# Kernel tuning notes

Hardware: AMD Instinct MI355X
Metric: run time of the kernel (lower is better)

## Reference

```python
import jax, jax.numpy as jnp
import numpy as np

B, S, D = 8, 1024, 1024
H, DK = 16, 64  # heads, key_size (== head_size)
NEG = 1e12


def setup_inputs() -> dict:
    key = jax.random.key(0)
    ks = jax.random.split(key, 10)
    s = 1.0 / np.sqrt(D)
    return {
        "q": jax.random.normal(ks[0], (B, S, D), jnp.float32),
        "k": jax.random.normal(ks[1], (B, S, D), jnp.float32),
        "v": jax.random.normal(ks[2], (B, S, D), jnp.float32),
        "pos_bias": jax.random.normal(ks[3], (S, S, DK), jnp.float32) * 0.02,
        "Wq": jax.random.normal(ks[4], (D, H * DK), jnp.float32) * s,
        "Wk": jax.random.normal(ks[5], (D, H * DK), jnp.float32) * s,
        "Wv": jax.random.normal(ks[6], (D, H * DK), jnp.float32) * s,
        "Wo": jax.random.normal(ks[7], (H * DK, D), jnp.float32) * s,
        "bq": jnp.zeros((H * DK,), jnp.float32),
        "bk": jnp.zeros((H * DK,), jnp.float32),
        "bv": jnp.zeros((H * DK,), jnp.float32),
        "bo": jnp.zeros((D,), jnp.float32),
        "q_mask": jnp.ones((B, S), jnp.int32),
        "v_mask": jnp.ones((B, S), jnp.int32),
    }


def reference(q, k, v, pos_bias, Wq, Wk, Wv, Wo, bq, bk, bv, bo, q_mask, v_mask):
    qm = q_mask.astype(q.dtype)  # [B,Sq]
    vm = v_mask.astype(q.dtype)  # [B,Sk]
    # Projections (faithful quirk: K is projected from v, as in the source)
    qw = (q @ Wq + bq).reshape(B, S, H, DK)
    kw = (v @ Wk + bk).reshape(B, S, H, DK)
    vw = (v @ Wv + bv).reshape(B, S, H, DK)
    # scores + inline relative-position bias ('typial_relative' branch)
    a = jnp.einsum('bjhd,bkhd->bhjk', qw, kw)
    a = a + jnp.einsum('bjhd,jkd->bhjk', qw, pos_bias)
    a = a / jnp.sqrt(jnp.asarray(DK, a.dtype))
    # additive key mask, then softmax over keys
    a = a - (1.0 - vm)[:, None, None, :] * NEG
    a = jax.nn.softmax(a, axis=-1)
    o = jnp.einsum('bhjk,bkhd->bjhd', a, vw)  # [B,Sq,H,DK]
    o = o.reshape(B, S, H * DK) @ Wo + bo
    # multiplicative query mask on output
    o = o * qm[:, :, None]
    return o
```

## Files before the change

### kernel.cpp

```cpp
#include <hip/hip_runtime.h>

using short8 = __attribute__((ext_vector_type(8))) short;
using f32x4  = __attribute__((ext_vector_type(4))) float;
using u16x4  = __attribute__((ext_vector_type(4))) unsigned short;
using fl4    = __attribute__((ext_vector_type(4))) float;

#define MFMA16(a, b, c) __builtin_amdgcn_mfma_f32_16x16x32_bf16((a), (b), (c), 0, 0, 0)

static __device__ __forceinline__ unsigned short f2bf(float f) {
  union { float f; unsigned u; } x; x.f = f;
  return (unsigned short)((x.u + 0x7FFFu + ((x.u >> 16) & 1u)) >> 16);
}
static __device__ __forceinline__ float bf2f(unsigned short s) {
  union { unsigned u; float f; } x; x.u = ((unsigned)s) << 16;
  return x.f;
}

static __device__ __forceinline__ void gload16(const void* g, void* l) {
  __builtin_amdgcn_global_load_lds((const __attribute__((address_space(1))) void*)g,
                                   (__attribute__((address_space(3))) void*)l, 16, 0, 0);
}

__global__ __launch_bounds__(256) void k_wconv4(
    const float* __restrict__ W0, const float* __restrict__ W1,
    const float* __restrict__ W2, const float* __restrict__ W3,
    unsigned short* __restrict__ Wt0, unsigned short* __restrict__ Wt1,
    unsigned short* __restrict__ Wt2, unsigned short* __restrict__ Wt3) {
  const float* W = (blockIdx.z == 0) ? W0 : (blockIdx.z == 1) ? W1
                   : (blockIdx.z == 2) ? W2 : W3;
  unsigned short* Wt = (blockIdx.z == 0) ? Wt0 : (blockIdx.z == 1) ? Wt1
                       : (blockIdx.z == 2) ? Wt2 : Wt3;
  __shared__ float tile[64][65];
  const int t = threadIdx.x;
  const int n0 = blockIdx.x * 64, k0 = blockIdx.y * 64;
#pragma unroll
  for (int p = 0; p < 4; ++p) {
    int row = p * 16 + (t >> 4);
    int c4 = (t & 15) * 4;
    fl4 val = *(const fl4*)&W[(size_t)(k0 + row) * 1024 + n0 + c4];
    tile[row][c4 + 0] = val[0];
    tile[row][c4 + 1] = val[1];
    tile[row][c4 + 2] = val[2];
    tile[row][c4 + 3] = val[3];
  }
  __syncthreads();
#pragma unroll
  for (int p = 0; p < 4; ++p) {
    int n = p * 16 + (t >> 4);
    int k4 = (t & 15) * 4;
    u16x4 u;
    u[0] = f2bf(tile[k4 + 0][n]);
    u[1] = f2bf(tile[k4 + 1][n]);
    u[2] = f2bf(tile[k4 + 2][n]);
    u[3] = f2bf(tile[k4 + 3][n]);
    *(u16x4*)&Wt[(size_t)(n0 + n) * 1024 + k0 + k4] = u;
  }
}

__global__ __launch_bounds__(256) void k_cvt(const float* __restrict__ a,
                                             const float* __restrict__ b,
                                             unsigned short* __restrict__ oa,
                                             unsigned short* __restrict__ ob) {
  const float* src = blockIdx.y ? b : a;
  unsigned short* dst = blockIdx.y ? ob : oa;
  size_t i = ((size_t)blockIdx.x * 256 + threadIdx.x) * 8;
  fl4 v0 = *(const fl4*)&src[i];
  fl4 v1 = *(const fl4*)&src[i + 4];
  u16x4 u0, u1;
  u0[0] = f2bf(v0[0]); u0[1] = f2bf(v0[1]); u0[2] = f2bf(v0[2]); u0[3] = f2bf(v0[3]);
  u1[0] = f2bf(v1[0]); u1[1] = f2bf(v1[1]); u1[2] = f2bf(v1[2]); u1[3] = f2bf(v1[3]);
  *(u16x4*)&dst[i] = u0;
  *(u16x4*)&dst[i + 4] = u1;
}

__global__ __launch_bounds__(256) void k_proj2(
    const unsigned short* __restrict__ QB, const unsigned short* __restrict__ VB,
    const unsigned short* __restrict__ WtQ, const unsigned short* __restrict__ WtK,
    const unsigned short* __restrict__ WtV,
    const float* __restrict__ bq, const float* __restrict__ bk,
    const float* __restrict__ bv,
    unsigned short* __restrict__ QW, unsigned short* __restrict__ KW,
    unsigned short* __restrict__ VWT) {
  const int mode = blockIdx.z;
  const unsigned short* A8 = (mode == 0) ? QB : VB;
  const unsigned short* Wt = (mode == 0) ? WtQ : (mode == 1) ? WtK : WtV;
  const float* bias = (mode == 0) ? bq : (mode == 1) ? bk : bv;
  const int n0 = blockIdx.x * 128, m0 = blockIdx.y * 128;
  const int t = threadIdx.x, lane = t & 63, w = t >> 6;
  const int g = lane >> 4, ln = lane & 15;
  const int wm = w >> 1, wn = w & 1;
  __shared__ unsigned short sh[16896];
  unsigned short* As = sh;
  unsigned short* Bs = sh + 8192;
  const int srow = lane >> 3;
  const int scol = (lane & 7) * 8;
  f32x4 acc[4][4] = {};
  for (int kk = 0; kk < 1024; kk += 64) {
    __syncthreads();
#pragma unroll
    for (int p = 0; p < 4; ++p) {
      gload16(&A8[(size_t)(m0 + p * 32 + w * 8 + srow) * 1024 + kk + scol],
              &As[p * 2048 + w * 512]);
      gload16(&Wt[(size_t)(n0 + p * 32 + w * 8 + srow) * 1024 + kk + scol],
              &Bs[p * 2048 + w * 512]);
    }
    __syncthreads();
#pragma unroll
    for (int ks = 0; ks < 2; ++ks) {
      short8 af[4];
#pragma unroll
      for (int fm = 0; fm < 4; ++fm)
        af[fm] = *(const short8*)&As[(wm * 64 + fm * 16 + ln) * 64 + ks * 32 + 8 * g];
#pragma unroll
      for (int fn = 0; fn < 4; ++fn) {
        short8 bfr = *(const short8*)&Bs[(wn * 64 + fn * 16 + ln) * 64 + ks * 32 + 8 * g];
#pragma unroll
        for (int fm = 0; fm < 4; ++fm) acc[fm][fn] = MFMA16(af[fm], bfr, acc[fm][fn]);
      }
    }
  }
  __syncthreads();
  const float scale = (mode == 0) ? 0.125f : 1.0f;
#pragma unroll
  for (int fn = 0; fn < 4; ++fn) {
    float bn = bias[n0 + wn * 64 + fn * 16 + ln];
#pragma unroll
    for (int fm = 0; fm < 4; ++fm) {
#pragma unroll
      for (int r = 0; r < 4; ++r) {
        float val = (acc[fm][fn][r] + bn) * scale;
        sh[(wm * 64 + fm * 16 + 4 * g + r) * 132 + wn * 64 + fn * 16 + ln] = f2bf(val);
      }
    }
  }
  __syncthreads();
  if (mode < 2) {
    unsigned short* OUT = (mode == 0) ? QW : KW;
#pragma unroll
    for (int p = 0; p < 16; ++p) {
      int row = p * 8 + (t >> 5), c4 = (t & 31) * 4;
      *(u16x4*)&OUT[(size_t)(m0 + row) * 1024 + n0 + c4] =
          *(const u16x4*)&sh[row * 132 + c4];
    }
  } else {
    const int b = m0 >> 10, s0 = m0 & 1023;
#pragma unroll
    for (int p = 0; p < 16; ++p) {
#pragma unroll
      for (int qh = 0; qh < 2; ++qh) {
        int hdl = p * 8 + (t >> 5);
        int sl = qh * 64 + (t & 31) * 2;
        unsigned lo = sh[sl * 132 + hdl];
        unsigned hi = sh[(sl + 1) * 132 + hdl];
        int hd = n0 + hdl;
        int h = hd >> 6, d = hd & 63;
        *(unsigned*)&VWT[((size_t)(b * 16 + h) * 64 + d) * 1024 + s0 + sl] =
            lo | (hi << 16);
      }
    }
  }
}

__global__ __launch_bounds__(256) void k_pbias(
    const unsigned short* __restrict__ QW, const float* __restrict__ pb,
    const int* __restrict__ vmask, unsigned short* __restrict__ CB, int jbase) {
  const int kt = blockIdx.x;
  const int jl = blockIdx.y;
  const int j = jbase + jl;
  const int t = threadIdx.x, lane = t & 63, w = t >> 6;
  const int g = lane >> 4, ln = lane & 15;
  const int wm = w >> 1, wn = w & 1;
  __shared__ unsigned short sm[18432];
  unsigned short* a_lds = sm;
  unsigned short* b_lds = sm + 9216;
#pragma unroll
  for (int p = 0; p < 8; ++p) {
    int i4 = p * 256 + t;
    int row = i4 >> 4, c4 = (i4 & 15) * 4;
    *(u16x4*)&a_lds[row * 72 + c4] =
        *(const u16x4*)&QW[((size_t)(row >> 4) * 1024 + j) * 1024 + (row & 15) * 64 + c4];
  }
#pragma unroll
  for (int p = 0; p < 8; ++p) {
    int i4 = p * 256 + t;
    int row = i4 >> 4, c4 = (i4 & 15) * 4;
    fl4 val = *(const fl4*)&pb[((size_t)j * 1024 + kt * 128 + row) * 64 + c4];
    u16x4 u;
    u[0] = f2bf(val[0]); u[1] = f2bf(val[1]);
    u[2] = f2bf(val[2]); u[3] = f2bf(val[3]);
    *(u16x4*)&b_lds[row * 72 + c4] = u;
  }
  __syncthreads();
  f32x4 acc[4][4] = {};
#pragma unroll
  for (int ks = 0; ks < 2; ++ks) {
    short8 af[4];
#pragma unroll
    for (int fm = 0; fm < 4; ++fm)
      af[fm] = *(const short8*)&a_lds[(wm * 64 + fm * 16 + ln) * 72 + ks * 32 + 8 * g];
#pragma unroll
    for (int fn = 0; fn < 4; ++fn) {
      short8 bfr = *(const short8*)&b_lds[(wn * 64 + fn * 16 + ln) * 72 + ks * 32 + 8 * g];
#pragma unroll
      for (int fm = 0; fm < 4; ++fm) acc[fm][fn] = MFMA16(af[fm], bfr, acc[fm][fn]);
    }
  }
  __syncthreads();
#pragma unroll
  for (int fn = 0; fn < 4; ++fn) {
    int kcol = kt * 128 + wn * 64 + fn * 16 + ln;
#pragma unroll
    for (int fm = 0; fm < 4; ++fm) {
      float off = vmask[(wm * 4 + fm) * 1024 + kcol] ? 0.f : -1e12f;
#pragma unroll
      for (int r = 0; r < 4; ++r)
        sm[(wm * 64 + fm * 16 + 4 * g + r) * 132 + wn * 64 + fn * 16 + ln] =
            f2bf(acc[fm][fn][r] + off);
    }
  }
  __syncthreads();
#pragma unroll
  for (int p = 0; p < 16; ++p) {
    int row = p * 8 + (t >> 5), c4 = (t & 31) * 4;
    *(u16x4*)&CB[((size_t)row * 512 + jl) * 1024 + kt * 128 + c4] =
        *(const u16x4*)&sm[row * 132 + c4];
  }
}

__global__ __launch_bounds__(256) void k_attn(
    const unsigned short* __restrict__ QW, const unsigned short* __restrict__ KW,
    const unsigned short* __restrict__ VWT, const unsigned short* __restrict__ CB,
    unsigned short* __restrict__ OB, int jbase) {
  const int jt = blockIdx.x, h = blockIdx.y, b = blockIdx.z;
  const int t = threadIdx.x, lane = t & 63, w = t >> 6;
  const int g = lane >> 4, ln = lane & 15;
  const int j0 = jbase + jt * 64;
  const int jl0 = jt * 64;
  __shared__ unsigned short lds_k[128 * 72];
  __shared__ unsigned short lds_vt[64 * 136];
  __shared__ unsigned short lds_p[4 * 16 * 136];
  unsigned short* pw = &lds_p[w * (16 * 136)];
  short8 qf[2];
  {
    const size_t qrow = ((size_t)b * 1024 + (j0 + w * 16 + ln)) * 1024 + h * 64;
    qf[0] = *(const short8*)&QW[qrow + 8 * g];
    qf[1] = *(const short8*)&QW[qrow + 32 + 8 * g];
  }
  const size_t cb_row = ((size_t)(b * 16 + h) * 512 + jl0 + w * 16 + ln) * 1024;

  u16x4 rk[8], rv[8], rcb[8];
#define LOAD_KV(kt_)                                                              \
  {                                                                               \
    _Pragma("unroll") for (int p = 0; p < 8; ++p) {                               \
      int i4 = p * 256 + t;                                                       \
      int row = i4 >> 4, c4 = (i4 & 15) * 4;                                      \
      rk[p] = *(const u16x4*)&KW[((size_t)b * 1024 + (kt_) * 128 + row) * 1024 +  \
                                 h * 64 + c4];                                    \
    }                                                                             \
    _Pragma("unroll") for (int p = 0; p < 8; ++p) {                               \
      int i4 = p * 256 + t;                                                       \
      int row = i4 >> 5, c4 = (i4 & 31) * 4;                                      \
      rv[p] = *(const u16x4*)&VWT[(((size_t)b * 16 + h) * 64 + row) * 1024 +      \
                                  (kt_) * 128 + c4];                              \
    }                                                                             \
    _Pragma("unroll") for (int p = 0; p < 8; ++p)                                 \
        rcb[p] = *(const u16x4*)&CB[cb_row + (kt_) * 128 + p * 16 + 4 * g];       \
  }

  LOAD_KV(0);
  f32x4 o_acc[4] = {};
  float l_par = 0.f;

  for (int kt = 0; kt < 8; ++kt) {
    __syncthreads();
#pragma unroll
    for (int p = 0; p < 8; ++p) {
      int i4 = p * 256 + t;
      int row = i4 >> 4, c4 = (i4 & 15) * 4;
      *(u16x4*)&lds_k[row * 72 + c4] = rk[p];
    }
#pragma unroll
    for (int p = 0; p < 8; ++p) {
      int i4 = p * 256 + t;
      int row = i4 >> 5, c4 = (i4 & 31) * 4;
      *(u16x4*)&lds_vt[row * 136 + c4] = rv[p];
    }
    f32x4 s[8];
#pragma unroll
    for (int fm = 0; fm < 8; ++fm) {
#pragma unroll
      for (int r = 0; r < 4; ++r) s[fm][r] = bf2f(rcb[fm][r]);
    }
    if (kt < 7) LOAD_KV(kt + 1);
    __syncthreads();
#pragma unroll
    for (int ks = 0; ks < 2; ++ks) {
#pragma unroll
      for (int fm = 0; fm < 8; ++fm) {
        short8 af = *(const short8*)&lds_k[(fm * 16 + ln) * 72 + ks * 32 + 8 * g];
        s[fm] = MFMA16(af, qf[ks], s[fm]);
      }
    }
#pragma unroll
    for (int fm = 0; fm < 8; ++fm) {
      u16x4 pp;
#pragma unroll
      for (int r = 0; r < 4; ++r) {
        float pv = __expf(s[fm][r] - 12.0f);
        l_par += pv;
        pp[r] = f2bf(pv);
      }
      *(u16x4*)&pw[ln * 136 + fm * 16 + 4 * g] = pp;
    }
    asm volatile("s_waitcnt lgkmcnt(0)" ::: "memory");
#pragma unroll
    for (int ks = 0; ks < 4; ++ks) {
      short8 bp = *(const short8*)&pw[ln * 136 + ks * 32 + 8 * g];
#pragma unroll
      for (int fm = 0; fm < 4; ++fm) {
        short8 av = *(const short8*)&lds_vt[(fm * 16 + ln) * 136 + ks * 32 + 8 * g];
        o_acc[fm] = MFMA16(av, bp, o_acc[fm]);
      }
    }
  }
  l_par += __shfl_xor(l_par, 16);
  l_par += __shfl_xor(l_par, 32);
  float inv = 1.0f / l_par;
  const size_t orow = ((size_t)b * 1024 + (j0 + w * 16 + ln)) * 1024 + h * 64;
#pragma unroll
  for (int fm = 0; fm < 4; ++fm) {
    u16x4 uo;
#pragma unroll
    for (int r = 0; r < 4; ++r) uo[r] = f2bf(o_acc[fm][r] * inv);
    *(u16x4*)&OB[orow + fm * 16 + 4 * g] = uo;
  }
#undef LOAD_KV
}

__global__ __launch_bounds__(256) void k_out2(
    const unsigned short* __restrict__ OB, const unsigned short* __restrict__ WtO,
    const float* __restrict__ bo, const int* __restrict__ qmask,
    float* __restrict__ out) {
  const int n0 = blockIdx.x * 128, m0 = blockIdx.y * 128;
  const int t = threadIdx.x, lane = t & 63, w = t >> 6;
  const int g = lane >> 4, ln = lane & 15;
  const int wm = w >> 1, wn = w & 1;
  __shared__ unsigned short sh[16384];
  unsigned short* As = sh;
  unsigned short* Bs = sh + 8192;
  const int srow = lane >> 3;
  const int scol = (lane & 7) * 8;
  f32x4 acc[4][4] = {};
  for (int kk = 0; kk < 1024; kk += 64) {
    __syncthreads();
#pragma unroll
    for (int p = 0; p < 4; ++p) {
      gload16(&OB[(size_t)(m0 + p * 32 + w * 8 + srow) * 1024 + kk + scol],
              &As[p * 2048 + w * 512]);
      gload16(&WtO[(size_t)(n0 + p * 32 + w * 8 + srow) * 1024 + kk + scol],
              &Bs[p * 2048 + w * 512]);
    }
    __syncthreads();
#pragma unroll
    for (int ks = 0; ks < 2; ++ks) {
      short8 af[4];
#pragma unroll
      for (int fm = 0; fm < 4; ++fm)
        af[fm] = *(const short8*)&As[(wm * 64 + fm * 16 + ln) * 64 + ks * 32 + 8 * g];
#pragma unroll
      for (int fn = 0; fn < 4; ++fn) {
        short8 bfr = *(const short8*)&Bs[(wn * 64 + fn * 16 + ln) * 64 + ks * 32 + 8 * g];
#pragma unroll
        for (int fm = 0; fm < 4; ++fm) acc[fm][fn] = MFMA16(af[fm], bfr, acc[fm][fn]);
      }
    }
  }
  float bn[4];
#pragma unroll
  for (int fn = 0; fn < 4; ++fn) bn[fn] = bo[n0 + wn * 64 + fn * 16 + ln];
#pragma unroll
  for (int fm = 0; fm < 4; ++fm) {
#pragma unroll
    for (int r = 0; r < 4; ++r) {
      int row = m0 + wm * 64 + fm * 16 + 4 * g + r;
      float qm = (float)qmask[row];
#pragma unroll
      for (int fn = 0; fn < 4; ++fn)
        out[(size_t)row * 1024 + n0 + wn * 64 + fn * 16 + ln] =
            (acc[fm][fn][r] + bn[fn]) * qm;
    }
  }
}

extern "C" void kernel_launch(void* const* d_in, const int* in_sizes, int n_in,
                              void* d_out, int out_size, void* d_ws, size_t ws_size,
                              hipStream_t stream) {
  const float* q  = (const float*)d_in[0];
  const float* v  = (const float*)d_in[2];
  const float* pb = (const float*)d_in[3];
  const float* Wq = (const float*)d_in[4];
  const float* Wk = (const float*)d_in[5];
  const float* Wv = (const float*)d_in[6];
  const float* Wo = (const float*)d_in[7];
  const float* bq = (const float*)d_in[8];
  const float* bk = (const float*)d_in[9];
  const float* bv = (const float*)d_in[10];
  const float* bo = (const float*)d_in[11];
  const int* qm = (const int*)d_in[12];
  const int* vm = (const int*)d_in[13];
  float* out = (float*)d_out;

  unsigned short* ws = (unsigned short*)d_ws;
  const size_t M1 = 1024 * 1024;
  unsigned short* WTQ = ws;
  unsigned short* WTK = WTQ + M1;
  unsigned short* WTV = WTK + M1;
  unsigned short* WTO = WTV + M1;
  unsigned short* QB  = WTO + M1;
  unsigned short* VB  = QB + 8 * M1;
  unsigned short* QW  = VB + 8 * M1;
  unsigned short* KW  = QW + 8 * M1;
  unsigned short* VWT = KW + 8 * M1;
  unsigned short* OB  = VWT + 8 * M1;
  unsigned short* CB  = OB + 8 * M1;

  k_wconv4<<<dim3(16, 16, 4), 256, 0, stream>>>(Wq, Wk, Wv, Wo, WTQ, WTK, WTV, WTO);
  k_cvt<<<dim3(4096, 2), 256, 0, stream>>>(q, v, QB, VB);
  k_proj2<<<dim3(8, 64, 3), 256, 0, stream>>>(QB, VB, WTQ, WTK, WTV, bq, bk, bv,
                                              QW, KW, VWT);
  for (int st = 0; st < 2; ++st) {
    k_pbias<<<dim3(8, 512), 256, 0, stream>>>(QW, pb, vm, CB, st * 512);
    k_attn<<<dim3(8, 16, 8), 256, 0, stream>>>(QW, KW, VWT, CB, OB, st * 512);
  }
  k_out2<<<dim3(8, 64), 256, 0, stream>>>(OB, WTO, bo, qm, out);
}
```

Measured before the change: 390.4 us.

## Triple-buffer GEMM K-loop with swizzled LDS and use exp2 softmax

Replaces the synchronous two-barrier GEMM loop in the projection and output kernels with a shared macro. The macro keeps three LDS stages in flight through async global-to-LDS loads and uses vmcnt waits with one barrier per 32-wide K step, plus an XOR swizzle on LDS reads to reduce bank conflicts. The softmax now folds log2(e) into the Q scale and mask offset so it can call native v_exp_f32, and it uses packed bf16 conversion instructions. This adds LDS footprint, which may lower occupancy, and shifts the fixed softmax offset from 12 to 17 in the exp2 domain.

```diff
diff --git a/kernel.cpp b/kernel.cpp
--- a/kernel.cpp
+++ b/kernel.cpp
@@ -15,11 +15,20 @@
   union { unsigned u; float f; } x; x.u = ((unsigned)s) << 16;
   return x.f;
 }
+static __device__ __forceinline__ float fexp2(float x) {
+  float r; asm("v_exp_f32 %0, %1" : "=v"(r) : "v"(x)); return r;
+}
+static __device__ __forceinline__ unsigned pk2(float lo, float hi) {
+  unsigned r; asm("v_cvt_pk_bf16_f32 %0, %1, %2" : "=v"(r) : "v"(lo), "v"(hi));
+  return r;
+}
 
 static __device__ __forceinline__ void gload16(const void* g, void* l) {
   __builtin_amdgcn_global_load_lds((const __attribute__((address_space(1))) void*)g,
                                    (__attribute__((address_space(3))) void*)l, 16, 0, 0);
 }
+
+#define LOG2E 1.4426950408889634f
 
 __global__ __launch_bounds__(256) void k_wconv4(
     const float* __restrict__ W0, const float* __restrict__ W1,
@@ -73,7 +82,58 @@
   *(u16x4*)&dst[i + 4] = u1;
 }
 
-__global__ __launch_bounds__(256) void k_proj2(
+#define GEMM3_CORE(APTR, BPTR)                                                  \
+  const int t = threadIdx.x, lane = t & 63, w = t >> 6;                         \
+  const int g = lane >> 4, ln = lane & 15;                                      \
+  const int wm = w >> 1, wn = w & 1;                                            \
+  __shared__ unsigned short sh[24576];    \
+  const int srow = lane >> 2;                                                   \
+  const int sc = (lane & 3) ^ ((lane >> 3) & 3);                                \
+  const int rsw = ((ln >> 1) & 3);                                              \
+  f32x4 acc[4][4] = {};                                                         \
+  _Pragma("unroll") for (int pre = 0; pre < 2; ++pre) {                         \
+    _Pragma("unroll") for (int p = 0; p < 2; ++p) {                             \
+      gload16(&APTR[(size_t)(m0 + p * 64 + w * 16 + srow) * 1024 + pre * 32 + sc * 8], \
+              &sh[pre * 8192 + (p * 64 + w * 16) * 32]);                        \
+      gload16(&BPTR[(size_t)(n0 + p * 64 + w * 16 + srow) * 1024 + pre * 32 + sc * 8], \
+              &sh[pre * 8192 + 4096 + (p * 64 + w * 16) * 32]);                 \
+    }                                                                           \
+  }                                                                             \
+  int cur = 0;                                                                  \
+  for (int tt = 0; tt < 32; ++tt) {                                             \
+    if (tt < 31) {                                                              \
+      asm volatile("s_waitcnt vmcnt(4)" ::: "memory");                          \
+    } else {                                                                    \
+      asm volatile("s_waitcnt vmcnt(0)" ::: "memory");                          \
+    }                                                                           \
+    __builtin_amdgcn_sched_barrier(0);                                          \
+    __builtin_amdgcn_s_barrier();                                               \
+    __builtin_amdgcn_sched_barrier(0);                                          \
+    if (tt < 30) {                                                              \
+      int bb = cur + 2; if (bb >= 3) bb -= 3;                                   \
+      int kk = (tt + 2) * 32;                                                   \
+      _Pragma("unroll") for (int p = 0; p < 2; ++p) {                           \
+        gload16(&APTR[(size_t)(m0 + p * 64 + w * 16 + srow) * 1024 + kk + sc * 8], \
+                &sh[bb * 8192 + (p * 64 + w * 16) * 32]);                       \
+        gload16(&BPTR[(size_t)(n0 + p * 64 + w * 16 + srow) * 1024 + kk + sc * 8], \
+                &sh[bb * 8192 + 4096 + (p * 64 + w * 16) * 32]);                \
+      }                                                                         \
+    }                                                                           \
+    const unsigned short* As = &sh[cur * 8192];                                 \
+    const unsigned short* Bs = As + 4096;                                       \
+    short8 af[4], bfr[4];                                                       \
+    _Pragma("unroll") for (int fm = 0; fm < 4; ++fm)                            \
+        af[fm] = *(const short8*)&As[(wm * 64 + fm * 16 + ln) * 32 + (g ^ rsw) * 8]; \
+    _Pragma("unroll") for (int fn = 0; fn < 4; ++fn)                            \
+        bfr[fn] = *(const short8*)&Bs[(wn * 64 + fn * 16 + ln) * 32 + (g ^ rsw) * 8]; \
+    _Pragma("unroll") for (int fn = 0; fn < 4; ++fn) {                          \
+      _Pragma("unroll") for (int fm = 0; fm < 4; ++fm)                          \
+          acc[fm][fn] = MFMA16(af[fm], bfr[fn], acc[fm][fn]);                   \
+    }                                                                           \
+    cur = (cur == 2) ? 0 : cur + 1;                                             \
+  }
+
+__global__ __launch_bounds__(256) void k_proj3(
     const unsigned short* __restrict__ QB, const unsigned short* __restrict__ VB,
     const unsigned short* __restrict__ WtQ, const unsigned short* __restrict__ WtK,
     const unsigned short* __restrict__ WtV,
@@ -86,41 +146,9 @@
   const unsigned short* Wt = (mode == 0) ? WtQ : (mode == 1) ? WtK : WtV;
   const float* bias = (mode == 0) ? bq : (mode == 1) ? bk : bv;
   const int n0 = blockIdx.x * 128, m0 = blockIdx.y * 128;
-  const int t = threadIdx.x, lane = t & 63, w = t >> 6;
-  const int g = lane >> 4, ln = lane & 15;
-  const int wm = w >> 1, wn = w & 1;
-  __shared__ unsigned short sh[16896];
-  unsigned short* As = sh;
-  unsigned short* Bs = sh + 8192;
-  const int srow = lane >> 3;
-  const int scol = (lane & 7) * 8;
-  f32x4 acc[4][4] = {};
-  for (int kk = 0; kk < 1024; kk += 64) {
-    __syncthreads();
-#pragma unroll
-    for (int p = 0; p < 4; ++p) {
-      gload16(&A8[(size_t)(m0 + p * 32 + w * 8 + srow) * 1024 + kk + scol],
-              &As[p * 2048 + w * 512]);
-      gload16(&Wt[(size_t)(n0 + p * 32 + w * 8 + srow) * 1024 + kk + scol],
-              &Bs[p * 2048 + w * 512]);
-    }
-    __syncthreads();
-#pragma unroll
-    for (int ks = 0; ks < 2; ++ks) {
-      short8 af[4];
-#pragma unroll
-      for (int fm = 0; fm < 4; ++fm)
-        af[fm] = *(const short8*)&As[(wm * 64 + fm * 16 + ln) * 64 + ks * 32 + 8 * g];
-#pragma unroll
-      for (int fn = 0; fn < 4; ++fn) {
-        short8 bfr = *(const short8*)&Bs[(wn * 64 + fn * 16 + ln) * 64 + ks * 32 + 8 * g];
-#pragma unroll
-        for (int fm = 0; fm < 4; ++fm) acc[fm][fn] = MFMA16(af[fm], bfr, acc[fm][fn]);
-      }
-    }
-  }
-  __syncthreads();
-  const float scale = (mode == 0) ? 0.125f : 1.0f;
+  GEMM3_CORE(A8, Wt)
+  __syncthreads();
+  const float scale = (mode == 0) ? (0.125f * LOG2E) : 1.0f;
 #pragma unroll
   for (int fn = 0; fn < 4; ++fn) {
     float bn = bias[n0 + wn * 64 + fn * 16 + ln];
@@ -157,6 +185,29 @@
         *(unsigned*)&VWT[((size_t)(b * 16 + h) * 64 + d) * 1024 + s0 + sl] =
             lo | (hi << 16);
       }
+    }
+  }
+}
+
+__global__ __launch_bounds__(256) void k_out3(
+    const unsigned short* __restrict__ OB, const unsigned short* __restrict__ WtO,
+    const float* __restrict__ bo, const int* __restrict__ qmask,
+    float* __restrict__ out) {
+  const int n0 = blockIdx.x * 128, m0 = blockIdx.y * 128;
+  GEMM3_CORE(OB, WtO)
+  float bn[4];
+#pragma unroll
+  for (int fn = 0; fn < 4; ++fn) bn[fn] = bo[n0 + wn * 64 + fn * 16 + ln];
+#pragma unroll
+  for (int fm = 0; fm < 4; ++fm) {
+#pragma unroll
+    for (int r = 0; r < 4; ++r) {
+      int row = m0 + wm * 64 + fm * 16 + 4 * g + r;
+      float qm = (float)qmask[row];
+#pragma unroll
+      for (int fn = 0; fn < 4; ++fn)
+        out[(size_t)row * 1024 + n0 + wn * 64 + fn * 16 + ln] =
+            (acc[fm][fn][r] + bn[fn]) * qm;
     }
   }
 }
@@ -211,7 +262,7 @@
     int kcol = kt * 128 + wn * 64 + fn * 16 + ln;
 #pragma unroll
     for (int fm = 0; fm < 4; ++fm) {
-      float off = vmask[(wm * 4 + fm) * 1024 + kcol] ? 0.f : -1e12f;
+      float off = vmask[(wm * 4 + fm) * 1024 + kcol] ? 0.f : (-1e12f * LOG2E);
 #pragma unroll
       for (int r = 0; r < 4; ++r)
         sm[(wm * 64 + fm * 16 + 4 * g + r) * 132 + wn * 64 + fn * 16 + ln] =
@@ -303,14 +354,15 @@
     }
 #pragma unroll
     for (int fm = 0; fm < 8; ++fm) {
-      u16x4 pp;
-#pragma unroll
-      for (int r = 0; r < 4; ++r) {
-        float pv = __expf(s[fm][r] - 12.0f);
-        l_par += pv;
-        pp[r] = f2bf(pv);
-      }
-      *(u16x4*)&pw[ln * 136 + fm * 16 + 4 * g] = pp;
+      float pv0 = fexp2(s[fm][0] - 17.0f);
+      float pv1 = fexp2(s[fm][1] - 17.0f);
+      float pv2 = fexp2(s[fm][2] - 17.0f);
+      float pv3 = fexp2(s[fm][3] - 17.0f);
+      l_par += (pv0 + pv1) + (pv2 + pv3);
+      union { u16x4 v; unsigned u[2]; } pp;
+      pp.u[0] = pk2(pv0, pv1);
+      pp.u[1] = pk2(pv2, pv3);
+      *(u16x4*)&pw[ln * 136 + fm * 16 + 4 * g] = pp.v;
     }
     asm volatile("s_waitcnt lgkmcnt(0)" ::: "memory");
 #pragma unroll
@@ -329,67 +381,12 @@
   const size_t orow = ((size_t)b * 1024 + (j0 + w * 16 + ln)) * 1024 + h * 64;
 #pragma unroll
   for (int fm = 0; fm < 4; ++fm) {
-    u16x4 uo;
-#pragma unroll
-    for (int r = 0; r < 4; ++r) uo[r] = f2bf(o_acc[fm][r] * inv);
-    *(u16x4*)&OB[orow + fm * 16 + 4 * g] = uo;
+    union { u16x4 v; unsigned u[2]; } uo;
+    uo.u[0] = pk2(o_acc[fm][0] * inv, o_acc[fm][1] * inv);
+    uo.u[1] = pk2(o_acc[fm][2] * inv, o_acc[fm][3] * inv);
+    *(u16x4*)&OB[orow + fm * 16 + 4 * g] = uo.v;
   }
 #undef LOAD_KV
-}
-
-__global__ __launch_bounds__(256) void k_out2(
-    const unsigned short* __restrict__ OB, const unsigned short* __restrict__ WtO,
-    const float* __restrict__ bo, const int* __restrict__ qmask,
-    float* __restrict__ out) {
-  const int n0 = blockIdx.x * 128, m0 = blockIdx.y * 128;
-  const int t = threadIdx.x, lane = t & 63, w = t >> 6;
-  const int g = lane >> 4, ln = lane & 15;
-  const int wm = w >> 1, wn = w & 1;
-  __shared__ unsigned short sh[16384];
-  unsigned short* As = sh;
-  unsigned short* Bs = sh + 8192;
-  const int srow = lane >> 3;
-  const int scol = (lane & 7) * 8;
-  f32x4 acc[4][4] = {};
-  for (int kk = 0; kk < 1024; kk += 64) {
-    __syncthreads();
-#pragma unroll
-    for (int p = 0; p < 4; ++p) {
-      gload16(&OB[(size_t)(m0 + p * 32 + w * 8 + srow) * 1024 + kk + scol],
-              &As[p * 2048 + w * 512]);
-      gload16(&WtO[(size_t)(n0 + p * 32 + w * 8 + srow) * 1024 + kk + scol],
-              &Bs[p * 2048 + w * 512]);
-    }
-    __syncthreads();
-#pragma unroll
-    for (int ks = 0; ks < 2; ++ks) {
-      short8 af[4];
-#pragma unroll
-      for (int fm = 0; fm < 4; ++fm)
-        af[fm] = *(const short8*)&As[(wm * 64 + fm * 16 + ln) * 64 + ks * 32 + 8 * g];
-#pragma unroll
-      for (int fn = 0; fn < 4; ++fn) {
-        short8 bfr = *(const short8*)&Bs[(wn * 64 + fn * 16 + ln) * 64 + ks * 32 + 8 * g];
-#pragma unroll
-        for (int fm = 0; fm < 4; ++fm) acc[fm][fn] = MFMA16(af[fm], bfr, acc[fm][fn]);
-      }
-    }
-  }
-  float bn[4];
-#pragma unroll
-  for (int fn = 0; fn < 4; ++fn) bn[fn] = bo[n0 + wn * 64 + fn * 16 + ln];
-#pragma unroll
-  for (int fm = 0; fm < 4; ++fm) {
-#pragma unroll
-    for (int r = 0; r < 4; ++r) {
-      int row = m0 + wm * 64 + fm * 16 + 4 * g + r;
-      float qm = (float)qmask[row];
-#pragma unroll
-      for (int fn = 0; fn < 4; ++fn)
-        out[(size_t)row * 1024 + n0 + wn * 64 + fn * 16 + ln] =
-            (acc[fm][fn][r] + bn[fn]) * qm;
-    }
-  }
 }
 
 extern "C" void kernel_launch(void* const* d_in, const int* in_sizes, int n_in,
@@ -426,11 +423,11 @@
 
   k_wconv4<<<dim3(16, 16, 4), 256, 0, stream>>>(Wq, Wk, Wv, Wo, WTQ, WTK, WTV, WTO);
   k_cvt<<<dim3(4096, 2), 256, 0, stream>>>(q, v, QB, VB);
-  k_proj2<<<dim3(8, 64, 3), 256, 0, stream>>>(QB, VB, WTQ, WTK, WTV, bq, bk, bv,
+  k_proj3<<<dim3(8, 64, 3), 256, 0, stream>>>(QB, VB, WTQ, WTK, WTV, bq, bk, bv,
                                               QW, KW, VWT);
   for (int st = 0; st < 2; ++st) {
     k_pbias<<<dim3(8, 512), 256, 0, stream>>>(QW, pb, vm, CB, st * 512);
     k_attn<<<dim3(8, 16, 8), 256, 0, stream>>>(QW, KW, VWT, CB, OB, st * 512);
   }
-  k_out2<<<dim3(8, 64), 256, 0, stream>>>(OB, WTO, bo, qm, out);
-}
+  k_out3<<<dim3(8, 64), 256, 0, stream>>>(OB, WTO, bo, qm, out);
+}
```

Measured after the change: 386.4 us. No clear change (-1.0%).
